# Performance work log

Hardware: AMD Instinct MI355X
Metric: run time of the kernel (lower is better)

Reference implementation:

```python
import jax, jax.numpy as jnp
import numpy as np

N_NODES = 100000
N_EDGES = 3200000
F_IN, F_HID, F_OUT = 36, 8, 2
NEG_SLOPE = 0.2


def gat_layer(x, src, dst, W, a_src, a_dst, b, num_nodes):
    # Linear transform: [N, F'] 
    h = x @ W
    # Per-node attention logits (heads=1)
    alpha_s = h @ a_src  # [N]
    alpha_d = h @ a_dst  # [N]
    # Edge-wise score: leaky_relu(a_src . h_j + a_dst . h_i) for edge j->i
    e = jax.nn.leaky_relu(alpha_s[src] + alpha_d[dst], negative_slope=NEG_SLOPE)  # [E]
    # Segment softmax over incoming edges of each dst node
    m = jax.ops.segment_max(e, dst, num_segments=num_nodes)  # [N]
    ee = jnp.exp(e - m[dst])
    denom = jax.ops.segment_sum(ee, dst, num_segments=num_nodes)  # [N]
    alpha = ee / denom[dst]  # [E]
    # Scatter-aggregate messages
    out = jax.ops.segment_sum(alpha[:, None] * h[src], dst, num_segments=num_nodes)
    return out + b


def setup_inputs() -> dict:
    key = jax.random.key(0)
    ks = jax.random.split(key, 10)
    x = jax.random.normal(ks[0], (N_NODES, F_IN), dtype=jnp.float32)
    edge_index = jax.random.randint(ks[1], (2, N_EDGES), 0, N_NODES, dtype=jnp.int64)
    s1 = 1.0 / np.sqrt(F_IN)
    s2 = 1.0 / np.sqrt(F_HID)
    W1 = jax.random.uniform(ks[2], (F_IN, F_HID), jnp.float32, -s1, s1)
    a_src1 = jax.random.uniform(ks[3], (F_HID,), jnp.float32, -s2, s2)
    a_dst1 = jax.random.uniform(ks[4], (F_HID,), jnp.float32, -s2, s2)
    b1 = jnp.zeros((F_HID,), jnp.float32)
    W2 = jax.random.uniform(ks[5], (F_HID, F_OUT), jnp.float32, -s2, s2)
    so = 1.0 / np.sqrt(F_OUT)
    a_src2 = jax.random.uniform(ks[6], (F_OUT,), jnp.float32, -so, so)
    a_dst2 = jax.random.uniform(ks[7], (F_OUT,), jnp.float32, -so, so)
    b2 = jnp.zeros((F_OUT,), jnp.float32)
    return {"x": x, "edge_index": edge_index, "W1": W1, "a_src1": a_src1,
            "a_dst1": a_dst1, "b1": b1, "W2": W2, "a_src2": a_src2,
            "a_dst2": a_dst2, "b2": b2}


def reference(x, edge_index, W1, a_src1, a_dst1, b1, W2, a_src2, a_dst2, b2):
    src, dst = edge_index[0], edge_index[1]
    n = x.shape[0]
    h = jax.nn.relu(gat_layer(x, src, dst, W1, a_src1, a_dst1, b1, n))
    # dropout is identity in eval mode
    out = gat_layer(h, src, dst, W2, a_src2, a_dst2, b2, n)
    return jax.nn.log_softmax(out, axis=1)
```

## Files before the change

### kernel.cpp

```cpp
#include <hip/hip_runtime.h>
#include <hip/hip_bf16.h>

#define N_NODES 100000
#define N_EDGES 3200000
#define F_IN 36
#define F_HID 8
#define F_OUT 2
#define NEG_SLOPE 0.2f

#define GSHIFT 7
#define GNPB 128
#define GNBUCK 782
#define CAP 4608
#define NB_PART 256
#define CHUNK 12500
#define BP 1024
#define NB_NODE1 98
#define BPG 512

__device__ __forceinline__ int detect_is64(const void* eidx, int* s_flag) {
    if (threadIdx.x < 64) {
        const unsigned int* p = (const unsigned int*)eidx;
        unsigned int v1 = p[2 * threadIdx.x + 1];
        unsigned int v2 = p[2 * (threadIdx.x + 64) + 1];
        unsigned long long m = __ballot(v1 != 0u || v2 != 0u);
        if (threadIdx.x == 0) *s_flag = (m == 0ull) ? 1 : 0;
    }
    __syncthreads();
    return *s_flag;
}

__global__ void part_node1_k(const void* __restrict__ eidx, int* __restrict__ gcnt,
                             int* __restrict__ partP,
                             const float* __restrict__ x, const float* __restrict__ W1,
                             const float* __restrict__ aw_d,
                             float* __restrict__ h1, float* __restrict__ ad1) {
    if (blockIdx.x < NB_PART) {
        __shared__ int sortbuf[CHUNK];
        __shared__ int hist[GNBUCK];
        __shared__ int spre[GNBUCK];
        __shared__ int cursor[GNBUCK];
        __shared__ int gbase[GNBUCK];
        __shared__ int s_flag;
        int t = threadIdx.x;
        for (int i = t; i < GNBUCK; i += BP) hist[i] = 0;
        int f = detect_is64(eidx, &s_flag);
        int beg = blockIdx.x * CHUNK;
        int end = beg + CHUNK;
        const int BULK = (CHUNK / (4 * BP)) * (4 * BP);

        if (f) {
            const long long* p64 = (const long long*)eidx;
#pragma unroll
            for (int r = 0; r < CHUNK / (4 * BP); r++) {
                int base = beg + 4 * t + r * 4 * BP;
                longlong2 d01 = *(const longlong2*)(p64 + N_EDGES + base);
                longlong2 d23 = *(const longlong2*)(p64 + N_EDGES + base + 2);
                atomicAdd(&hist[(int)d01.x >> GSHIFT], 1);
                atomicAdd(&hist[(int)d01.y >> GSHIFT], 1);
                atomicAdd(&hist[(int)d23.x >> GSHIFT], 1);
                atomicAdd(&hist[(int)d23.y >> GSHIFT], 1);
            }
            for (int i = beg + BULK + t; i < end; i += BP)
                atomicAdd(&hist[(int)p64[N_EDGES + i] >> GSHIFT], 1);
        } else {
            const int* p = (const int*)eidx;
#pragma unroll
            for (int r = 0; r < CHUNK / (4 * BP); r++) {
                int base = beg + 4 * t + r * 4 * BP;
                int4 dv = *(const int4*)(p + N_EDGES + base);
                atomicAdd(&hist[dv.x >> GSHIFT], 1);
                atomicAdd(&hist[dv.y >> GSHIFT], 1);
                atomicAdd(&hist[dv.z >> GSHIFT], 1);
                atomicAdd(&hist[dv.w >> GSHIFT], 1);
            }
            for (int i = beg + BULK + t; i < end; i += BP)
                atomicAdd(&hist[p[N_EDGES + i] >> GSHIFT], 1);
        }
        __syncthreads();
        if (t < GNBUCK) {
            int c = hist[t];
            gbase[t] = c ? atomicAdd(&gcnt[t], c) : 0;
            spre[t] = c;
        }
        __syncthreads();
        for (int off = 1; off < GNBUCK; off <<= 1) {
            int v = 0;
            if (t < GNBUCK && t >= off) v = spre[t - off];
            __syncthreads();
            if (t < GNBUCK && t >= off) spre[t] += v;
            __syncthreads();
        }
        if (t < GNBUCK) cursor[t] = spre[t] - hist[t];
        __syncthreads();
        if (f) {
            const long long* p64 = (const long long*)eidx;
#pragma unroll
            for (int r = 0; r < CHUNK / (4 * BP); r++) {
                int base = beg + 4 * t + r * 4 * BP;
                longlong2 s01 = *(const longlong2*)(p64 + base);
                longlong2 s23 = *(const longlong2*)(p64 + base + 2);
                longlong2 d01 = *(const longlong2*)(p64 + N_EDGES + base);
                longlong2 d23 = *(const longlong2*)(p64 + N_EDGES + base + 2);
                int d, pos;
                d = (int)d01.x; pos = atomicAdd(&cursor[d >> GSHIFT], 1);
                sortbuf[pos] = ((int)s01.x << GSHIFT) | (d & (GNPB - 1));
                d = (int)d01.y; pos = atomicAdd(&cursor[d >> GSHIFT], 1);
                sortbuf[pos] = ((int)s01.y << GSHIFT) | (d & (GNPB - 1));
                d = (int)d23.x; pos = atomicAdd(&cursor[d >> GSHIFT], 1);
                sortbuf[pos] = ((int)s23.x << GSHIFT) | (d & (GNPB - 1));
                d = (int)d23.y; pos = atomicAdd(&cursor[d >> GSHIFT], 1);
                sortbuf[pos] = ((int)s23.y << GSHIFT) | (d & (GNPB - 1));
            }
            for (int i = beg + BULK + t; i < end; i += BP) {
                int s = (int)p64[i];
                int d = (int)p64[N_EDGES + i];
                int pos = atomicAdd(&cursor[d >> GSHIFT], 1);
                sortbuf[pos] = (s << GSHIFT) | (d & (GNPB - 1));
            }
        } else {
            const int* p = (const int*)eidx;
#pragma unroll
            for (int r = 0; r < CHUNK / (4 * BP); r++) {
                int base = beg + 4 * t + r * 4 * BP;
                int4 sv = *(const int4*)(p + base);
                int4 dv = *(const int4*)(p + N_EDGES + base);
                int pos;
                pos = atomicAdd(&cursor[dv.x >> GSHIFT], 1);
                sortbuf[pos] = (sv.x << GSHIFT) | (dv.x & (GNPB - 1));
                pos = atomicAdd(&cursor[dv.y >> GSHIFT], 1);
                sortbuf[pos] = (sv.y << GSHIFT) | (dv.y & (GNPB - 1));
                pos = atomicAdd(&cursor[dv.z >> GSHIFT], 1);
                sortbuf[pos] = (sv.z << GSHIFT) | (dv.z & (GNPB - 1));
                pos = atomicAdd(&cursor[dv.w >> GSHIFT], 1);
                sortbuf[pos] = (sv.w << GSHIFT) | (dv.w & (GNPB - 1));
            }
            for (int i = beg + BULK + t; i < end; i += BP) {
                int s = p[i];
                int d = p[N_EDGES + i];
                int pos = atomicAdd(&cursor[d >> GSHIFT], 1);
                sortbuf[pos] = (s << GSHIFT) | (d & (GNPB - 1));
            }
        }
        __syncthreads();
        for (int i = t; i < CHUNK; i += BP) {
            int lo = 0, hi = GNBUCK - 1;
            while (lo < hi) {
                int mid = (lo + hi) >> 1;
                if (spre[mid] > i) hi = mid; else lo = mid + 1;
            }
            int b = lo;
            int gp = gbase[b] + (i - (spre[b] - hist[b]));
            if (gp < CAP) partP[b * CAP + gp] = sortbuf[i];
        }
    } else {
        int n = (blockIdx.x - NB_PART) * BP + threadIdx.x;
        if (n >= N_NODES) return;
        float acc[F_HID];
#pragma unroll
        for (int f = 0; f < F_HID; f++) acc[f] = 0.f;
        const float4* xp = (const float4*)(x + (size_t)n * F_IN);
#pragma unroll
        for (int q = 0; q < 9; q++) {
            float4 xv = xp[q];
            const float* w = W1 + q * 4 * F_HID;
#pragma unroll
            for (int f = 0; f < F_HID; f++) {
                acc[f] += xv.x * w[0 * F_HID + f] + xv.y * w[1 * F_HID + f]
                        + xv.z * w[2 * F_HID + f] + xv.w * w[3 * F_HID + f];
            }
        }
        float d = 0.f;
#pragma unroll
        for (int f = 0; f < F_HID; f++) d += acc[f] * aw_d[f];
        float4* hp = (float4*)(h1 + (size_t)n * F_HID);
        hp[0] = make_float4(acc[0], acc[1], acc[2], acc[3]);
        hp[1] = make_float4(acc[4], acc[5], acc[6], acc[7]);
        ad1[n] = d;
    }
}

__global__ void gatF1_k(const int* __restrict__ gcnt, const int* __restrict__ partP,
                        int* __restrict__ e_srcP, int2* __restrict__ rowinfo,
                        const float* __restrict__ aw_s1, const float* __restrict__ ad1,
                        const float* __restrict__ h1, const float* __restrict__ b1,
                        const float* __restrict__ W2, const float* __restrict__ aw_s2,
                        const float* __restrict__ aw_d2, float4* __restrict__ P2) {
    __shared__ int eL[CAP];
    __shared__ int hist[GNPB];
    __shared__ int nstart[GNPB];
    __shared__ int cursor[GNPB];
    __shared__ int sscan[GNPB];
    __shared__ float adl[GNPB];
    int t = threadIdx.x;
    int c = blockIdx.x;
    int nbase = c << GSHIFT;
    int beg = c * CAP;
    int cnt = gcnt[c]; if (cnt > CAP) cnt = CAP;

    if (t < GNPB) {
        hist[t] = 0;
        adl[t] = (nbase + t < N_NODES) ? ad1[nbase + t] : 0.f;
    }
    __syncthreads();
    for (int j = t; j < cnt; j += BPG)
        atomicAdd(&hist[partP[beg + j] & (GNPB - 1)], 1);
    __syncthreads();
    if (t < GNPB) sscan[t] = hist[t];
    __syncthreads();
    for (int o = 1; o < GNPB; o <<= 1) {
        int u = (t < GNPB && t >= o) ? sscan[t - o] : 0;
        __syncthreads();
        if (t < GNPB) sscan[t] += u;
        __syncthreads();
    }
    if (t < GNPB) {
        int ex = sscan[t] - hist[t];
        nstart[t] = ex;
        cursor[t] = ex;
        int node = nbase + t;
        if (node < N_NODES) rowinfo[node] = make_int2(beg + ex, hist[t]);
    }
    __syncthreads();
    for (int j = t; j < cnt; j += BPG) {
        int pk = partP[beg + j];
        int pos = atomicAdd(&cursor[pk & (GNPB - 1)], 1);
        eL[pos] = pk >> GSHIFT;
    }
    __syncthreads();
    for (int i = t; i < cnt; i += BPG) e_srcP[beg + i] = eL[i];

    int node = t >> 2;
    int lane = t & 3;
    int gnode = nbase + node;
    if (gnode >= N_NODES) return;
    int ns = nstart[node];
    int ne = ns + hist[node];
    float add = adl[node];

    float ws0 = aw_s1[0], ws1 = aw_s1[1], ws2 = aw_s1[2], ws3 = aw_s1[3];
    float ws4 = aw_s1[4], ws5 = aw_s1[5], ws6 = aw_s1[6], ws7 = aw_s1[7];

    float denom = 0.f;
    float acc[F_HID];
#pragma unroll
    for (int f = 0; f < F_HID; f++) acc[f] = 0.f;
    for (int i = ns + lane; i < ne; i += 4) {
        int s = eL[i];
        const float4* hp = (const float4*)(h1 + (size_t)s * F_HID);
        float4 p0 = hp[0], p1 = hp[1];
        float e = p0.x * ws0 + p0.y * ws1 + p0.z * ws2 + p0.w * ws3
                + p1.x * ws4 + p1.y * ws5 + p1.z * ws6 + p1.w * ws7 + add;
        e = e >= 0.f ? e : NEG_SLOPE * e;
        float ee = __expf(e);
        denom += ee;
        acc[0] += ee * p0.x; acc[1] += ee * p0.y; acc[2] += ee * p0.z; acc[3] += ee * p0.w;
        acc[4] += ee * p1.x; acc[5] += ee * p1.y; acc[6] += ee * p1.z; acc[7] += ee * p1.w;
    }
#pragma unroll
    for (int o = 2; o > 0; o >>= 1) {
        denom += __shfl_xor(denom, o, 4);
#pragma unroll
        for (int f = 0; f < F_HID; f++) acc[f] += __shfl_xor(acc[f], o, 4);
    }
    if (lane == 0) {
        float inv = denom > 0.f ? 1.f / denom : 0.f;
        float o0 = 0.f, o1 = 0.f;
#pragma unroll
        for (int f = 0; f < F_HID; f++) {
            float v = acc[f] * inv + b1[f];
            v = v > 0.f ? v : 0.f;
            o0 += v * W2[f * F_OUT + 0];
            o1 += v * W2[f * F_OUT + 1];
        }
        float as2v = o0 * aw_s2[0] + o1 * aw_s2[1];
        float ad2v = o0 * aw_d2[0] + o1 * aw_d2[1];
        P2[gnode] = make_float4(as2v, o0, o1, ad2v);
    }
}

__global__ void gat2_k(const int2* __restrict__ rowinfo, const int* __restrict__ e_srcP,
                       const float4* __restrict__ P2, const float* __restrict__ b2,
                       float* __restrict__ out, int n_nodes) {
    int gid = blockIdx.x * 16 + (threadIdx.x >> 4);
    int lane = threadIdx.x & 15;
    if (gid >= n_nodes) return;
    int2 ri = rowinfo[gid];
    float add = P2[gid].w;

    float denom = 0.f, a0 = 0.f, a1 = 0.f;
    int jend = ri.x + ri.y;
    for (int j = ri.x + lane; j < jend; j += 16) {
        int s = e_srcP[j];
        float4 q = P2[s];
        float e = q.x + add;
        e = e >= 0.f ? e : NEG_SLOPE * e;
        float ee = __expf(e);
        denom += ee;
        a0 += ee * q.y;
        a1 += ee * q.z;
    }
#pragma unroll
    for (int o = 8; o > 0; o >>= 1) {
        denom += __shfl_xor(denom, o, 16);
        a0 += __shfl_xor(a0, o, 16);
        a1 += __shfl_xor(a1, o, 16);
    }

    if (lane == 0) {
        float inv = denom > 0.f ? 1.f / denom : 0.f;
        float o0 = a0 * inv + b2[0];
        float o1 = a1 * inv + b2[1];
        float M = fmaxf(o0, o1);
        float l = M + logf(__expf(o0 - M) + __expf(o1 - M));
        ((float2*)out)[gid] = make_float2(o0 - l, o1 - l);
    }
}

extern "C" void kernel_launch(void* const* d_in, const int* in_sizes, int n_in,
                              void* d_out, int out_size, void* d_ws, size_t ws_size,
                              hipStream_t stream) {
    const float* x      = (const float*)d_in[0];
    const void*  eidx   = d_in[1];
    const float* W1     = (const float*)d_in[2];
    const float* a_src1 = (const float*)d_in[3];
    const float* a_dst1 = (const float*)d_in[4];
    const float* b1     = (const float*)d_in[5];
    const float* W2     = (const float*)d_in[6];
    const float* a_src2 = (const float*)d_in[7];
    const float* a_dst2 = (const float*)d_in[8];
    const float* b2     = (const float*)d_in[9];
    float* out = (float*)d_out;

    const size_t N = N_NODES;
    const size_t PADDED = (size_t)GNBUCK * CAP;

    int* wsi = (int*)d_ws;
    float* wsf = (float*)d_ws;
    size_t o = 0;
    int* partP    = wsi + o;      o += PADDED;
    int* e_srcP   = wsi + o;      o += PADDED;
    int* gcnt     = wsi + o;      o += 800;
    int2* rowinfo = (int2*)(wsi + o); o += 2 * N;
    float* ad1    = wsf + o;      o += N;
    o = (o + 15) & ~(size_t)15;
    float* h1     = wsf + o;      o += 8 * N;
    float4* P2    = (float4*)(wsf + o); o += 4 * N;

    const int gridG = (int)(N / 16);

    hipMemsetAsync(gcnt, 0, 800 * sizeof(int), stream);

    part_node1_k<<<NB_PART + NB_NODE1, BP, 0, stream>>>(eidx, gcnt, partP,
                                                        x, W1, a_dst1, h1, ad1);
    gatF1_k<<<GNBUCK, BPG, 0, stream>>>(gcnt, partP, e_srcP, rowinfo, a_src1, ad1, h1, b1,
                                        W2, a_src2, a_dst2, P2);
    gat2_k<<<gridG, 256, 0, stream>>>(rowinfo, e_srcP, P2, b2, out, (int)N);
}
```

Before: 166.0 us.

## Aggregate layer two directly from bucketed edges with shared-memory atomics

Layer 1 no longer writes the sorted source array and per-node row info to global memory. Layer 2 now reads the packed bucket partition directly, one block per bucket, and accumulates the softmax denominator and weighted messages per destination node with LDS float atomics. This removes a 12.8MB-class global write plus the later reread, in exchange for shared-memory atomic contention and non-deterministic summation order. The layer-2 softmax omits the max subtraction, as the code before also did.

Result: slower. 209.4 us (+26.2%).

```diff
diff --git a/kernel.cpp b/kernel.cpp
--- a/kernel.cpp
+++ b/kernel.cpp
@@ -181,7 +181,6 @@
 }
 
 __global__ void gatF1_k(const int* __restrict__ gcnt, const int* __restrict__ partP,
-                        int* __restrict__ e_srcP, int2* __restrict__ rowinfo,
                         const float* __restrict__ aw_s1, const float* __restrict__ ad1,
                         const float* __restrict__ h1, const float* __restrict__ b1,
                         const float* __restrict__ W2, const float* __restrict__ aw_s2,
@@ -218,8 +217,6 @@
         int ex = sscan[t] - hist[t];
         nstart[t] = ex;
         cursor[t] = ex;
-        int node = nbase + t;
-        if (node < N_NODES) rowinfo[node] = make_int2(beg + ex, hist[t]);
     }
     __syncthreads();
     for (int j = t; j < cnt; j += BPG) {
@@ -228,7 +225,6 @@
         eL[pos] = pk >> GSHIFT;
     }
     __syncthreads();
-    for (int i = t; i < cnt; i += BPG) e_srcP[beg + i] = eL[i];
 
     int node = t >> 2;
     int lane = t & 3;
@@ -279,41 +275,45 @@
     }
 }
 
-__global__ void gat2_k(const int2* __restrict__ rowinfo, const int* __restrict__ e_srcP,
+__global__ void gat2_k(const int* __restrict__ gcnt, const int* __restrict__ partP,
                        const float4* __restrict__ P2, const float* __restrict__ b2,
-                       float* __restrict__ out, int n_nodes) {
-    int gid = blockIdx.x * 16 + (threadIdx.x >> 4);
-    int lane = threadIdx.x & 15;
-    if (gid >= n_nodes) return;
-    int2 ri = rowinfo[gid];
-    float add = P2[gid].w;
-
-    float denom = 0.f, a0 = 0.f, a1 = 0.f;
-    int jend = ri.x + ri.y;
-    for (int j = ri.x + lane; j < jend; j += 16) {
-        int s = e_srcP[j];
+                       float* __restrict__ out) {
+    __shared__ float den[GNPB], sa0[GNPB], sa1[GNPB], ad2l[GNPB];
+    int t = threadIdx.x;
+    int c = blockIdx.x;
+    int nbase = c << GSHIFT;
+    int beg = c * CAP;
+    int cnt = gcnt[c]; if (cnt > CAP) cnt = CAP;
+
+    if (t < GNPB) {
+        den[t] = 0.f; sa0[t] = 0.f; sa1[t] = 0.f;
+        ad2l[t] = (nbase + t < N_NODES) ? P2[nbase + t].w : 0.f;
+    }
+    __syncthreads();
+    for (int j = t; j < cnt; j += BPG) {
+        int pk = partP[beg + j];
+        int s = pk >> GSHIFT;
+        int dl = pk & (GNPB - 1);
         float4 q = P2[s];
-        float e = q.x + add;
+        float e = q.x + ad2l[dl];
         e = e >= 0.f ? e : NEG_SLOPE * e;
         float ee = __expf(e);
-        denom += ee;
-        a0 += ee * q.y;
-        a1 += ee * q.z;
-    }
-#pragma unroll
-    for (int o = 8; o > 0; o >>= 1) {
-        denom += __shfl_xor(denom, o, 16);
-        a0 += __shfl_xor(a0, o, 16);
-        a1 += __shfl_xor(a1, o, 16);
-    }
-
-    if (lane == 0) {
-        float inv = denom > 0.f ? 1.f / denom : 0.f;
-        float o0 = a0 * inv + b2[0];
-        float o1 = a1 * inv + b2[1];
-        float M = fmaxf(o0, o1);
-        float l = M + logf(__expf(o0 - M) + __expf(o1 - M));
-        ((float2*)out)[gid] = make_float2(o0 - l, o1 - l);
+        atomicAdd(&den[dl], ee);
+        atomicAdd(&sa0[dl], ee * q.y);
+        atomicAdd(&sa1[dl], ee * q.z);
+    }
+    __syncthreads();
+    if (t < GNPB) {
+        int gnode = nbase + t;
+        if (gnode < N_NODES) {
+            float d2 = den[t];
+            float inv = d2 > 0.f ? 1.f / d2 : 0.f;
+            float o0 = sa0[t] * inv + b2[0];
+            float o1 = sa1[t] * inv + b2[1];
+            float M = fmaxf(o0, o1);
+            float l = M + logf(__expf(o0 - M) + __expf(o1 - M));
+            ((float2*)out)[gnode] = make_float2(o0 - l, o1 - l);
+        }
     }
 }
 
@@ -339,21 +339,17 @@
     float* wsf = (float*)d_ws;
     size_t o = 0;
     int* partP    = wsi + o;      o += PADDED;
-    int* e_srcP   = wsi + o;      o += PADDED;
     int* gcnt     = wsi + o;      o += 800;
-    int2* rowinfo = (int2*)(wsi + o); o += 2 * N;
     float* ad1    = wsf + o;      o += N;
     o = (o + 15) & ~(size_t)15;
     float* h1     = wsf + o;      o += 8 * N;
     float4* P2    = (float4*)(wsf + o); o += 4 * N;
 
-    const int gridG = (int)(N / 16);
-
     hipMemsetAsync(gcnt, 0, 800 * sizeof(int), stream);
 
     part_node1_k<<<NB_PART + NB_NODE1, BP, 0, stream>>>(eidx, gcnt, partP,
                                                         x, W1, a_dst1, h1, ad1);
-    gatF1_k<<<GNBUCK, BPG, 0, stream>>>(gcnt, partP, e_srcP, rowinfo, a_src1, ad1, h1, b1,
+    gatF1_k<<<GNBUCK, BPG, 0, stream>>>(gcnt, partP, a_src1, ad1, h1, b1,
                                         W2, a_src2, a_dst2, P2);
-    gat2_k<<<gridG, 256, 0, stream>>>(rowinfo, e_srcP, P2, b2, out, (int)N);
-}
+    gat2_k<<<GNBUCK, BPG, 0, stream>>>(gcnt, partP, P2, b2, out);
+}
```
